# Performance work log

Hardware: AMD Instinct MI355X
Metric: run time of the kernel (lower is better)

The kernel has to match this reference:

```python
import jax, jax.numpy as jnp
from jax import lax
import numpy as np

INPUT_DIM = 1024; ENT_DIM = 256; KEY_DIM = 32; FUNC_DIM = 256; HID = 32
NUM_LAYERS = 1; UNIT_TYPE_DIM = 259; MAX_ENT = 64; B = 256; N = 512
NEG = 1e9

def _ln(x, g, b, eps=1e-5):
    m = x.mean(-1, keepdims=True)
    v = ((x - m) ** 2).mean(-1, keepdims=True)
    return (x - m) / jnp.sqrt(v + eps) * g + b

def setup_inputs() -> dict:
    key = jax.random.key(0)
    ks = jax.random.split(key, 16)
    def lin(k, i, o, s=0.02):
        return jax.random.normal(k, (i, o), jnp.float32) * s, jnp.zeros((o,), jnp.float32)
    p = {}
    p['key_fc_w'], p['key_fc_b'] = lin(ks[0], ENT_DIM, KEY_DIM)
    p['func_fc_w'], p['func_fc_b'] = lin(ks[1], UNIT_TYPE_DIM, FUNC_DIM)
    p['fc1_w'], p['fc1_b'] = lin(ks[2], INPUT_DIM, FUNC_DIM)
    p['fc2_w'], p['fc2_b'] = lin(ks[3], FUNC_DIM, KEY_DIM)
    p['embed_fc_w'], p['embed_fc_b'] = lin(ks[4], KEY_DIM, INPUT_DIM)
    p['lstm_wx'] = jax.random.normal(ks[5], (NUM_LAYERS, KEY_DIM, 4 * HID), jnp.float32) * 0.05
    p['lstm_wh'] = jax.random.normal(ks[6], (NUM_LAYERS, HID, 4 * HID), jnp.float32) * 0.05
    p['lstm_b'] = jnp.zeros((NUM_LAYERS, 4 * HID), jnp.float32)
    p['lstm_ln_gx'] = jnp.ones((NUM_LAYERS, 4 * HID), jnp.float32)
    p['lstm_ln_bx'] = jnp.zeros((NUM_LAYERS, 4 * HID), jnp.float32)
    p['lstm_ln_gh'] = jnp.ones((NUM_LAYERS, 4 * HID), jnp.float32)
    p['lstm_ln_bh'] = jnp.zeros((NUM_LAYERS, 4 * HID), jnp.float32)
    inp = {
        'embedding': jax.random.normal(ks[7], (B, INPUT_DIM), jnp.float32),
        'available_unit_type_mask': (jax.random.uniform(ks[8], (B, UNIT_TYPE_DIM)) < 0.5).astype(jnp.float32),
        'available_units_mask': jnp.ones((B, N), jnp.float32),
        'entity_embedding': jax.random.normal(ks[9], (B, N, ENT_DIM), jnp.float32),
        'temperature': jnp.float32(1.0),
    }
    inp.update(p)
    return inp

def reference(embedding, available_unit_type_mask, available_units_mask, entity_embedding,
              temperature, key_fc_w, key_fc_b, func_fc_w, func_fc_b, fc1_w, fc1_b,
              fc2_w, fc2_b, embed_fc_w, embed_fc_b, lstm_wx, lstm_wh, lstm_b,
              lstm_ln_gx, lstm_ln_bx, lstm_ln_gh, lstm_ln_bh):
    relu = jax.nn.relu
    # _get_key: [B,N,KEY] + end-flag row of zeros -> [B,N+1,KEY]
    key = entity_embedding @ key_fc_w + key_fc_b
    key = jnp.concatenate([key, jnp.zeros((B, 1, KEY_DIM), key.dtype)], axis=1)
    end_idx = N
    # _get_init_query
    func_embed = relu(available_unit_type_mask @ func_fc_w + func_fc_b)
    x0 = relu(embedding @ fc1_w + fc1_b)
    x0 = relu((x0 + func_embed) @ fc2_w + fc2_b)  # [B, KEY_DIM]
    mask0 = jnp.concatenate([available_units_mask, jnp.ones((B, 1), available_units_mask.dtype)], axis=1)

    h0 = jnp.zeros((NUM_LAYERS, B, HID), key.dtype)
    c0 = jnp.zeros((NUM_LAYERS, B, HID), key.dtype)
    units0 = jnp.zeros((B, N + 1), jnp.int32)
    done0 = jnp.zeros((B,), bool)
    rng0 = jax.random.key(42)

    def step(carry, _):
        x, h, c, mask, units, done, rng = carry
        xi = x
        hs, cs = [], []
        for l in range(NUM_LAYERS):  # LN-LSTM, gate order i,f,o,u (DI-engine)
            gate = (_ln(xi @ lstm_wx[l], lstm_ln_gx[l], lstm_ln_bx[l])
                    + _ln(h[l] @ lstm_wh[l], lstm_ln_gh[l], lstm_ln_bh[l]) + lstm_b[l])
            i_g, f_g, o_g, u_g = jnp.split(gate, 4, axis=-1)
            cl = jax.nn.sigmoid(f_g) * c[l] + jax.nn.sigmoid(i_g) * jnp.tanh(u_g)
            hl = jax.nn.sigmoid(o_g) * jnp.tanh(cl)
            hs.append(hl); cs.append(cl); xi = hl
        h_new = jnp.stack(hs); c_new = jnp.stack(cs)
        q = (xi[:, None, :] * key).mean(-1)          # [B, N+1] pointer scores
        q = q - (1.0 - mask) * NEG
        rng, sk = jax.random.split(rng)
        idx = jax.random.categorical(sk, q / temperature, axis=-1)  # [B]
        is_end = idx == end_idx
        active = jnp.logical_not(done)
        sel = active & jnp.logical_not(is_end)
        onehot = jax.nn.one_hot(idx, N + 1, dtype=mask.dtype)
        units = jnp.where(sel[:, None] & (onehot > 0.5), 1, units)
        mask = jnp.where(sel[:, None], mask * (1.0 - onehot), mask)
        done = done | (active & is_end)
        return (xi, h_new, c_new, mask, units, done, rng), (q, active)

    carry, (logits, valid) = lax.scan(step, (x0, h0, c0, mask0, units0, done0, rng0), None, length=MAX_ENT)
    units = carry[4]
    emb_sel = (units[..., None].astype(key.dtype) * key).mean(axis=1)  # [B, KEY_DIM]
    emb_sel = emb_sel @ embed_fc_w + embed_fc_b
    return logits, valid, units, embedding + emb_sel
```

## Files before the change

kernel.cpp:

```cpp
#include <hip/hip_runtime.h>
#include <stdint.h>
#include <stddef.h>

#define JAX_PARTITIONABLE 1

#define B_   256
#define N_   512
#define NP_  513
#define KROW 516
#define T_   64
#define CS   4
#define NCH  16
#define NEGC 1e9f

__host__ __device__ __forceinline__ void tf2x32(uint32_t k0, uint32_t k1,
    uint32_t x0, uint32_t x1, uint32_t& o0, uint32_t& o1) {
  const uint32_t k2 = k0 ^ k1 ^ 0x1BD11BDAu;
#define TFR(r) { x0 += x1; x1 = (x1 << (r)) | (x1 >> (32 - (r))); x1 ^= x0; }
  x0 += k0; x1 += k1;
  TFR(13) TFR(15) TFR(26) TFR(6)
  x0 += k1; x1 += k2 + 1u;
  TFR(17) TFR(29) TFR(16) TFR(24)
  x0 += k2; x1 += k0 + 2u;
  TFR(13) TFR(15) TFR(26) TFR(6)
  x0 += k0; x1 += k1 + 3u;
  TFR(17) TFR(29) TFR(16) TFR(24)
  x0 += k1; x1 += k2 + 4u;
  TFR(13) TFR(15) TFR(26) TFR(6)
  x0 += k2; x1 += k0 + 5u;
#undef TFR
  o0 = x0; o1 = x1;
}

struct SkKeys { uint32_t k[128]; };

static SkKeys compute_chain() {
  SkKeys s;
  uint32_t r0 = 0u, r1 = 42u;
  for (int t = 0; t < 64; ++t) {
#if JAX_PARTITIONABLE
    uint32_t a0, a1, b0, b1;
    tf2x32(r0, r1, 0u, 0u, a0, a1);
    tf2x32(r0, r1, 0u, 1u, b0, b1);
    s.k[2*t] = b0; s.k[2*t+1] = b1;
    r0 = a0; r1 = a1;
#else
    uint32_t p0, p1, q0, q1;
    tf2x32(r0, r1, 0u, 2u, p0, p1);
    tf2x32(r0, r1, 1u, 3u, q0, q1);
    s.k[2*t] = p1; s.k[2*t+1] = q1;
    r0 = p0; r1 = q0;
#endif
  }
  return s;
}

__device__ __forceinline__ float gumbel_draw(uint32_t k0, uint32_t k1, int b, int n) {
  uint32_t bits;
#if JAX_PARTITIONABLE
  uint32_t j = (uint32_t)(b * NP_ + n);
  uint32_t o0, o1; tf2x32(k0, k1, 0u, j, o0, o1);
  bits = o0 ^ o1;
#else
  int j = b * NP_ + n;
  uint32_t o0, o1;
  if (j < 65664) { tf2x32(k0, k1, (uint32_t)j, (uint32_t)(j + 65664), o0, o1); bits = o0; }
  else           { tf2x32(k0, k1, (uint32_t)(j - 65664), (uint32_t)j, o0, o1); bits = o1; }
#endif
  float f = __uint_as_float((bits >> 9) | 0x3F800000u) - 1.0f;
  const float TINY = 1.17549435e-38f;
  float u = fmaxf(TINY, f + TINY);
  return -logf(-logf(u));
}

__device__ __forceinline__ float sigm(float x) {
  return 0.5f + 0.5f * tanhf(0.5f * x);
}

__device__ __forceinline__ void bar_lds() {
  asm volatile("s_waitcnt lgkmcnt(0)\n\ts_barrier" ::: "memory");
}

#define OFF_KEY   0
#define OFF_H     16512
#define OFF_Q     18560
#define OFF_G     22688
#define OFF_UNITS 33008
#define OFF_SK    33524
#define OFF_ES    33652
#define OFF_PART  33684
#define OFF_T     34196
#define OFF_X0    34452
#define LDS_FLOATS 34484

__global__ void __launch_bounds__(512, 1)
suh_fused(const float* __restrict__ emb, const float* __restrict__ autm,
          const float* __restrict__ aum, const float* __restrict__ ent,
          const float* __restrict__ temp_p,
          const float* __restrict__ key_w, const float* __restrict__ key_b,
          const float* __restrict__ func_w, const float* __restrict__ func_b,
          const float* __restrict__ fc1_w, const float* __restrict__ fc1_b,
          const float* __restrict__ fc2_w, const float* __restrict__ fc2_b,
          const float* __restrict__ emb_w, const float* __restrict__ emb_b,
          const float* __restrict__ wx, const float* __restrict__ wh,
          const float* __restrict__ lstm_bb,
          const float* __restrict__ ln_gx, const float* __restrict__ ln_bx,
          const float* __restrict__ ln_gh, const float* __restrict__ ln_bh,
          float* __restrict__ out_logits, float* __restrict__ out_valid,
          float* __restrict__ out_units, float* __restrict__ out_final,
          SkKeys sk)
{
  extern __shared__ __align__(16) float sm[];
  int* smi = (int*)sm;
  const int b   = blockIdx.x;
  const int tid = threadIdx.x;
  const int L   = tid - 64;

  const float temp = temp_p[0];

  if (tid < 256) {
    float a = 0.f;
    const float* e = emb + (size_t)b * 1024;
    #pragma unroll 8
    for (int k = 0; k < 1024; ++k) a += e[k] * fc1_w[k * 256 + tid];
    a = fmaxf(a + fc1_b[tid], 0.f);
    float f = 0.f;
    const float* m = autm + (size_t)b * 259;
    for (int k = 0; k < 259; ++k) f += m[k] * func_w[k * 256 + tid];
    f = fmaxf(f + func_b[tid], 0.f);
    sm[OFF_T + tid] = a + f;
  } else {
    if (tid < 384) smi[OFF_SK + (tid - 256)] = (int)sk.k[tid - 256];
    if (tid >= 480) sm[OFF_KEY + (tid - 480) * KROW + N_] = 0.f;
  }
  __syncthreads();

  if (tid < 32) {
    float s = 0.f;
    #pragma unroll 8
    for (int m2 = 0; m2 < 256; ++m2) s += sm[OFF_T + m2] * fc2_w[m2 * 32 + tid];
    sm[OFF_X0 + tid] = fmaxf(s + fc2_b[tid], 0.f);
  }
  __syncthreads();

  float kr0[32], kr1[32];
  float mreg[8], ureg[8];
  float m512 = 1.0f;
  int done_reg = 0;

  auto qprep = [&](int cc, int qs) {
    const int qb = OFF_Q + qs * (CS * 516);
    #pragma unroll 1
    for (int tl = 0; tl < CS; ++tl) {
      const int hb = OFF_H + (cc * CS + tl) * 32;
      float hv[32];
      #pragma unroll
      for (int r = 0; r < 8; ++r) {
        float4 v = *(const float4*)&sm[hb + r * 4];
        hv[r*4] = v.x; hv[r*4+1] = v.y; hv[r*4+2] = v.z; hv[r*4+3] = v.w;
      }
      float a0 = 0.f;
      #pragma unroll
      for (int k = 0; k < 32; ++k) a0 += hv[k] * kr0[k];
      sm[qb + tl * 516 + L] = a0 * (1.0f / 32.0f);
      if (L < 64) {
        float a1 = 0.f;
        #pragma unroll
        for (int k = 0; k < 32; ++k) a1 += hv[k] * kr1[k];
        sm[qb + tl * 516 + L + 448] = a1 * (1.0f / 32.0f);
      }
    }
  };
  auto gprep = [&](int cc, int gs) {
    const int gb = OFF_G + gs * (CS * 516);
    #pragma unroll 1
    for (int i = 0; i < 5; ++i) {
      const int idx = i * 448 + L;
      if (idx < CS * 512) {
        const int tl = idx >> 9, n = idx & 511;
        const int t = cc * CS + tl;
        sm[gb + tl * 516 + n] =
            gumbel_draw((uint32_t)smi[OFF_SK + 2*t], (uint32_t)smi[OFF_SK + 2*t + 1], b, n);
      }
    }
    if (L < CS) {
      const int t = cc * CS + L;
      sm[gb + L * 516 + N_] =
          gumbel_draw((uint32_t)smi[OFF_SK + 2*t], (uint32_t)smi[OFF_SK + 2*t + 1], b, N_);
    }
  };

  if (tid < 64) {
    float wxr0[32], wxr1[32], whr0[32], whr1[32];
    #pragma unroll
    for (int k = 0; k < 32; ++k) {
      wxr0[k] = wx[k * 128 + tid];
      wxr1[k] = wx[k * 128 + 64 + tid];
      whr0[k] = wh[k * 128 + tid];
      whr1[k] = wh[k * 128 + 64 + tid];
    }
    const float gxg0 = ln_gx[tid], gxg1 = ln_gx[tid + 64];
    const float gxb0 = ln_bx[tid], gxb1 = ln_bx[tid + 64];
    const float ghg0 = ln_gh[tid], ghg1 = ln_gh[tid + 64];
    const float ghb0 = ln_bh[tid], ghb1 = ln_bh[tid + 64];
    const float lb0  = lstm_bb[tid], lb1 = lstm_bb[tid + 64];

    float xf[32];
    #pragma unroll
    for (int r = 0; r < 8; ++r) {
      float4 v = *(const float4*)&sm[OFF_X0 + r * 4];
      xf[r*4] = v.x; xf[r*4+1] = v.y; xf[r*4+2] = v.z; xf[r*4+3] = v.w;
    }
    float creg = 0.f;

    #pragma unroll 1
    for (int t = 0; t < T_; ++t) {
      #pragma unroll
      for (int k = 0; k < 32; ++k) {
        asm volatile("" : "+v"(wxr0[k]), "+v"(wxr1[k]), "+v"(whr0[k]), "+v"(whr1[k]));
      }
      float a0 = 0.f, a1 = 0.f, b0 = 0.f, b1 = 0.f;
      #pragma unroll
      for (int k = 0; k < 32; ++k) { a0 += xf[k] * wxr0[k]; a1 += xf[k] * wxr1[k]; }
      if (t > 0) {
        #pragma unroll
        for (int k = 0; k < 32; ++k) { b0 += xf[k] * whr0[k]; b1 += xf[k] * whr1[k]; }
      }
      float sx = a0 + a1, sh = b0 + b1;
      for (int off = 32; off; off >>= 1) {
        sx += __shfl_down(sx, off);
        sh += __shfl_down(sh, off);
      }
      float mx  = __shfl(sx, 0) * (1.0f / 128.0f);
      float mh2 = __shfl(sh, 0) * (1.0f / 128.0f);
      float dx0 = a0 - mx, dx1 = a1 - mx;
      float dh0 = b0 - mh2, dh1 = b1 - mh2;
      float ssx = dx0 * dx0 + dx1 * dx1;
      float ssh = dh0 * dh0 + dh1 * dh1;
      for (int off = 32; off; off >>= 1) {
        ssx += __shfl_down(ssx, off);
        ssh += __shfl_down(ssh, off);
      }
      float vx = __shfl(ssx, 0) * (1.0f / 128.0f);
      float vh = __shfl(ssh, 0) * (1.0f / 128.0f);
      float rx = 1.0f / sqrtf(vx + 1e-5f);
      float rh = 1.0f / sqrtf(vh + 1e-5f);
      float lnx0 = dx0 * rx * gxg0 + gxb0;
      float lnx1 = dx1 * rx * gxg1 + gxb1;
      float lnh0 = dh0 * rh * ghg0 + ghb0;
      float lnh1 = dh1 * rh * ghg1 + ghb1;
      float g0 = lnx0 + lnh0 + lb0;
      float g1 = lnx1 + lnh1 + lb1;
      float fq = __shfl(g0, tid + 32);
      float uq = __shfl(g1, tid + 32);
      float cN = sigm(fq) * creg + sigm(g0) * tanhf(uq);
      float hN = sigm(g1) * tanhf(cN);
      creg = cN;
      if (tid < 32) sm[OFF_H + t * 32 + tid] = hN;
      #pragma unroll
      for (int k = 0; k < 32; ++k) xf[k] = __shfl(hN, k);
    }
  } else {
    const float4* kw4 = (const float4*)key_w;
    {
      const float4* er = (const float4*)(ent + ((size_t)b * N_ + L) * 256);
      float acc[32];
      #pragma unroll
      for (int c = 0; c < 32; ++c) acc[c] = 0.f;
      #pragma unroll 4
      for (int k4 = 0; k4 < 64; ++k4) {
        float4 ev = er[k4];
        float e4[4] = {ev.x, ev.y, ev.z, ev.w};
        #pragma unroll
        for (int j = 0; j < 4; ++j) {
          const int k = k4 * 4 + j;
          #pragma unroll
          for (int c4 = 0; c4 < 8; ++c4) {
            float4 w = kw4[k * 8 + c4];
            acc[c4*4+0] += e4[j] * w.x;
            acc[c4*4+1] += e4[j] * w.y;
            acc[c4*4+2] += e4[j] * w.z;
            acc[c4*4+3] += e4[j] * w.w;
          }
        }
      }
      #pragma unroll
      for (int c = 0; c < 32; ++c) {
        kr0[c] = acc[c] + key_b[c];
        sm[OFF_KEY + c * KROW + L] = kr0[c];
      }
    }
    if (L < 64) {
      const int n = L + 448;
      const float4* er = (const float4*)(ent + ((size_t)b * N_ + n) * 256);
      float acc[32];
      #pragma unroll
      for (int c = 0; c < 32; ++c) acc[c] = 0.f;
      #pragma unroll 4
      for (int k4 = 0; k4 < 64; ++k4) {
        float4 ev = er[k4];
        float e4[4] = {ev.x, ev.y, ev.z, ev.w};
        #pragma unroll
        for (int j = 0; j < 4; ++j) {
          const int k = k4 * 4 + j;
          #pragma unroll
          for (int c4 = 0; c4 < 8; ++c4) {
            float4 w = kw4[k * 8 + c4];
            acc[c4*4+0] += e4[j] * w.x;
            acc[c4*4+1] += e4[j] * w.y;
            acc[c4*4+2] += e4[j] * w.z;
            acc[c4*4+3] += e4[j] * w.w;
          }
        }
      }
      #pragma unroll
      for (int c = 0; c < 32; ++c) {
        kr1[c] = acc[c] + key_b[c];
        sm[OFF_KEY + c * KROW + n] = kr1[c];
      }
    }
    #pragma unroll
    for (int k = 0; k < 32; ++k) {
      asm volatile("" : "+v"(kr0[k]), "+v"(kr1[k]));
    }
    #pragma unroll 1
    for (int cc = 0; cc < 4; ++cc) gprep(cc, cc);
  }
  __syncthreads();

  if (tid < 64) {
    #pragma unroll
    for (int j = 0; j < 8; ++j) {
      mreg[j] = aum[(size_t)b * N_ + tid + 64 * j];
      ureg[j] = 0.f;
    }
  } else {
    qprep(0, 0);
  }
  bar_lds();

  for (int c = 0; c < NCH; ++c) {
    if (tid < 64) {
      const int qbase = OFF_Q + (c & 1) * (CS * 516);
      const int gbase = OFF_G + (c % 5) * (CS * 516);
      #pragma unroll 1
      for (int tl = 0; tl < CS; ++tl) {
        const int t = c * CS + tl;
        float* lrow = out_logits + ((size_t)t * B_ + b) * NP_;
        float bv = 0.f; int bi = 0;
        #pragma unroll
        for (int j = 0; j < 8; ++j) {
          const int n = tid + 64 * j;
          float q = sm[qbase + tl * 516 + n] - (1.0f - mreg[j]) * NEGC;
          lrow[n] = q;
          float v = q / temp + sm[gbase + tl * 516 + n];
          if (j == 0) { bv = v; bi = n; }
          else if (v > bv) { bv = v; bi = n; }
        }
        if (tid == 0) {
          float q = -(1.0f - m512) * NEGC;
          lrow[N_] = q;
          float v = q / temp + sm[gbase + tl * 516 + N_];
          if (v > bv) { bv = v; bi = N_; }
        }
        for (int off = 32; off; off >>= 1) {
          float ov = __shfl_down(bv, off);
          int   oi = __shfl_down(bi, off);
          if (ov > bv || (ov == bv && oi < bi)) { bv = ov; bi = oi; }
        }
        const int sel_i = __shfl(bi, 0);
        const int active = !done_reg;
        const int is_end = (sel_i == N_);
        if (tid == 0) out_valid[(size_t)t * B_ + b] = active ? 1.0f : 0.0f;
        if (active && !is_end) {
          #pragma unroll
          for (int j = 0; j < 8; ++j)
            if (tid + 64 * j == sel_i) { mreg[j] = 0.0f; ureg[j] = 1.0f; }
        }
        if (active && is_end) done_reg = 1;
      }
    } else {
      if (c + 1 < NCH) qprep(c + 1, (c + 1) & 1);
      if (c + 4 < NCH) gprep(c + 4, (c + 4) % 5);
    }
    bar_lds();
  }

  if (tid < 64) {
    #pragma unroll
    for (int j = 0; j < 8; ++j) sm[OFF_UNITS + tid + 64 * j] = ureg[j];
    if (tid == 0) sm[OFF_UNITS + N_] = 0.f;
  }
  __syncthreads();

  {
    const int g = tid >> 5, cc = tid & 31;
    float p = 0.f;
    const int n0 = g * 32;
    for (int nn = 0; nn < 32; ++nn) {
      const int n = n0 + nn;
      p += sm[OFF_UNITS + n] * sm[OFF_KEY + cc * KROW + n];
    }
    if (g == 15) p += sm[OFF_UNITS + N_] * sm[OFF_KEY + cc * KROW + N_];
    sm[OFF_PART + g * 32 + cc] = p;
  }
  for (int n = tid; n < NP_; n += 512) out_units[(size_t)b * NP_ + n] = sm[OFF_UNITS + n];
  __syncthreads();
  if (tid < 32) {
    float s = 0.f;
    #pragma unroll
    for (int g = 0; g < 16; ++g) s += sm[OFF_PART + g * 32 + tid];
    sm[OFF_ES + tid] = s / 513.0f;
  }
  __syncthreads();
  {
    const float* e = emb + (size_t)b * 1024;
    for (int d = tid; d < 1024; d += 512) {
      float a = 0.f;
      #pragma unroll
      for (int k = 0; k < 32; ++k) a += sm[OFF_ES + k] * emb_w[k * 1024 + d];
      out_final[(size_t)b * 1024 + d] = e[d] + a + emb_b[d];
    }
  }
}

extern "C" void kernel_launch(void* const* d_in, const int* in_sizes, int n_in,
                              void* d_out, int out_size, void* d_ws, size_t ws_size,
                              hipStream_t stream) {
  (void)in_sizes; (void)n_in; (void)d_ws; (void)ws_size; (void)out_size;
  const float* emb    = (const float*)d_in[0];
  const float* autm   = (const float*)d_in[1];
  const float* aum    = (const float*)d_in[2];
  const float* ent    = (const float*)d_in[3];
  const float* temp   = (const float*)d_in[4];
  const float* key_w  = (const float*)d_in[5];
  const float* key_b  = (const float*)d_in[6];
  const float* func_w = (const float*)d_in[7];
  const float* func_b = (const float*)d_in[8];
  const float* fc1_w  = (const float*)d_in[9];
  const float* fc1_b  = (const float*)d_in[10];
  const float* fc2_w  = (const float*)d_in[11];
  const float* fc2_b  = (const float*)d_in[12];
  const float* emb_w  = (const float*)d_in[13];
  const float* emb_b  = (const float*)d_in[14];
  const float* wx     = (const float*)d_in[15];
  const float* wh     = (const float*)d_in[16];
  const float* lb     = (const float*)d_in[17];
  const float* gxg    = (const float*)d_in[18];
  const float* gxb    = (const float*)d_in[19];
  const float* ghg    = (const float*)d_in[20];
  const float* ghb    = (const float*)d_in[21];
  float* out = (float*)d_out;

  const size_t OFF_V = (size_t)T_ * B_ * NP_;
  const size_t OFF_U = OFF_V + (size_t)T_ * B_;
  const size_t OFF_F = OFF_U + (size_t)B_ * NP_;

  SkKeys sk = compute_chain();

  suh_fused<<<dim3(B_), dim3(512), LDS_FLOATS * sizeof(float), stream>>>(
      emb, autm, aum, ent, temp, key_w, key_b, func_w, func_b,
      fc1_w, fc1_b, fc2_w, fc2_b, emb_w, emb_b,
      wx, wh, lb, gxg, gxb, ghg, ghb,
      out, out + OFF_V, out + OFF_U, out + OFF_F, sk);
}
```

Before: 250.9 us.

## Double chunk size, double-buffer gumbel prep, and use xor-shuffle allreduce in LSTM

The sampling steps are now grouped in chunks of 8 instead of 4, which halves the number of block barriers between the sampling wave and the producer waves. Gumbel-noise generation changes from a 5-slot, 4-chunk lookahead to a 2-slot double buffer that is filled together with the next chunk's scores. The LSTM layernorm reductions use xor-shuffle allreduces, which removes the separate broadcast shuffles. The per-step register pinning moves out of the recurrence loop into a one-time v_mov. In exchange, more LDS is used per chunk, and the first chunk's noise is less covered by prefetch.

```diff
diff --git a/kernel.cpp b/kernel.cpp
--- a/kernel.cpp
+++ b/kernel.cpp
@@ -9,8 +9,8 @@
 #define NP_  513
 #define KROW 516
 #define T_   64
-#define CS   4
-#define NCH  16
+#define CS   8
+#define NCH  8
 #define NEGC 1e9f
 
 __host__ __device__ __forceinline__ void tf2x32(uint32_t k0, uint32_t k1,
@@ -84,14 +84,14 @@
 #define OFF_KEY   0
 #define OFF_H     16512
 #define OFF_Q     18560
-#define OFF_G     22688
-#define OFF_UNITS 33008
-#define OFF_SK    33524
-#define OFF_ES    33652
-#define OFF_PART  33684
-#define OFF_T     34196
-#define OFF_X0    34452
-#define LDS_FLOATS 34484
+#define OFF_G     26816
+#define OFF_UNITS 35072
+#define OFF_SK    35588
+#define OFF_ES    35716
+#define OFF_PART  35748
+#define OFF_T     36260
+#define OFF_X0    36516
+#define LDS_FLOATS 36548
 
 __global__ void __launch_bounds__(512, 1)
 suh_fused(const float* __restrict__ emb, const float* __restrict__ autm,
@@ -174,7 +174,7 @@
   auto gprep = [&](int cc, int gs) {
     const int gb = OFF_G + gs * (CS * 516);
     #pragma unroll 1
-    for (int i = 0; i < 5; ++i) {
+    for (int i = 0; i < 10; ++i) {
       const int idx = i * 448 + L;
       if (idx < CS * 512) {
         const int tl = idx >> 9, n = idx & 511;
@@ -199,6 +199,13 @@
       whr0[k] = wh[k * 128 + tid];
       whr1[k] = wh[k * 128 + 64 + tid];
     }
+    #pragma unroll
+    for (int k = 0; k < 32; ++k) {
+      asm volatile("v_mov_b32 %0, %0" : "+v"(wxr0[k]));
+      asm volatile("v_mov_b32 %0, %0" : "+v"(wxr1[k]));
+      asm volatile("v_mov_b32 %0, %0" : "+v"(whr0[k]));
+      asm volatile("v_mov_b32 %0, %0" : "+v"(whr1[k]));
+    }
     const float gxg0 = ln_gx[tid], gxg1 = ln_gx[tid + 64];
     const float gxb0 = ln_bx[tid], gxb1 = ln_bx[tid + 64];
     const float ghg0 = ln_gh[tid], ghg1 = ln_gh[tid + 64];
@@ -215,10 +222,6 @@
 
     #pragma unroll 1
     for (int t = 0; t < T_; ++t) {
-      #pragma unroll
-      for (int k = 0; k < 32; ++k) {
-        asm volatile("" : "+v"(wxr0[k]), "+v"(wxr1[k]), "+v"(whr0[k]), "+v"(whr1[k]));
-      }
       float a0 = 0.f, a1 = 0.f, b0 = 0.f, b1 = 0.f;
       #pragma unroll
       for (int k = 0; k < 32; ++k) { a0 += xf[k] * wxr0[k]; a1 += xf[k] * wxr1[k]; }
@@ -228,21 +231,21 @@
       }
       float sx = a0 + a1, sh = b0 + b1;
       for (int off = 32; off; off >>= 1) {
-        sx += __shfl_down(sx, off);
-        sh += __shfl_down(sh, off);
-      }
-      float mx  = __shfl(sx, 0) * (1.0f / 128.0f);
-      float mh2 = __shfl(sh, 0) * (1.0f / 128.0f);
+        sx += __shfl_xor(sx, off);
+        sh += __shfl_xor(sh, off);
+      }
+      float mx  = sx * (1.0f / 128.0f);
+      float mh2 = sh * (1.0f / 128.0f);
       float dx0 = a0 - mx, dx1 = a1 - mx;
       float dh0 = b0 - mh2, dh1 = b1 - mh2;
       float ssx = dx0 * dx0 + dx1 * dx1;
       float ssh = dh0 * dh0 + dh1 * dh1;
       for (int off = 32; off; off >>= 1) {
-        ssx += __shfl_down(ssx, off);
-        ssh += __shfl_down(ssh, off);
-      }
-      float vx = __shfl(ssx, 0) * (1.0f / 128.0f);
-      float vh = __shfl(ssh, 0) * (1.0f / 128.0f);
+        ssx += __shfl_xor(ssx, off);
+        ssh += __shfl_xor(ssh, off);
+      }
+      float vx = ssx * (1.0f / 128.0f);
+      float vh = ssh * (1.0f / 128.0f);
       float rx = 1.0f / sqrtf(vx + 1e-5f);
       float rh = 1.0f / sqrtf(vh + 1e-5f);
       float lnx0 = dx0 * rx * gxg0 + gxb0;
@@ -323,8 +326,7 @@
     for (int k = 0; k < 32; ++k) {
       asm volatile("" : "+v"(kr0[k]), "+v"(kr1[k]));
     }
-    #pragma unroll 1
-    for (int cc = 0; cc < 4; ++cc) gprep(cc, cc);
+    gprep(0, 0);
   }
   __syncthreads();
 
@@ -342,7 +344,7 @@
   for (int c = 0; c < NCH; ++c) {
     if (tid < 64) {
       const int qbase = OFF_Q + (c & 1) * (CS * 516);
-      const int gbase = OFF_G + (c % 5) * (CS * 516);
+      const int gbase = OFF_G + (c & 1) * (CS * 516);
       #pragma unroll 1
       for (int tl = 0; tl < CS; ++tl) {
         const int t = c * CS + tl;
@@ -380,8 +382,10 @@
         if (active && is_end) done_reg = 1;
       }
     } else {
-      if (c + 1 < NCH) qprep(c + 1, (c + 1) & 1);
-      if (c + 4 < NCH) gprep(c + 4, (c + 4) % 5);
+      if (c + 1 < NCH) {
+        qprep(c + 1, (c + 1) & 1);
+        gprep(c + 1, (c + 1) & 1);
+      }
     }
     bar_lds();
   }
```

Result: no change. 246.2 us (-1.9%).
